# Optimization experiments

Hardware: AMD Instinct MI355X
Metric: run time of the kernel (lower is better)

Reference implementation:

```python
import jax, jax.numpy as jnp
import numpy as np

B, S, D = 2, 2048, 4096
NH, NKV = 32, 8
HD = D // NH          # 128
NREP = NH // NKV      # 4
SCALE = HD ** -0.5


def setup_inputs() -> dict:
    key = jax.random.key(0)
    kx, kq, kk, kv, ko = jax.random.split(key, 5)
    s = 0.02
    return {
        "x": jax.random.normal(kx, (B, S, D), dtype=jnp.float32),
        "wq": jax.random.normal(kq, (D, NH * HD), dtype=jnp.float32) * s,
        "wk": jax.random.normal(kk, (D, NKV * HD), dtype=jnp.float32) * s,
        "wv": jax.random.normal(kv, (D, NKV * HD), dtype=jnp.float32) * s,
        "wo": jax.random.normal(ko, (NH * HD, D), dtype=jnp.float32) * s,
    }


def reference(x, wq, wk, wv, wo):
    b, s, _ = x.shape
    q = (x @ wq).reshape(b, s, NH, HD)    # b s h d
    k = (x @ wk).reshape(b, s, NKV, HD)   # b s kv d
    v = (x @ wv).reshape(b, s, NKV, HD)
    # GQA: repeat kv heads to match query heads
    k = jnp.repeat(k, NREP, axis=2)       # b s h d
    v = jnp.repeat(v, NREP, axis=2)
    scores = jnp.einsum("bihd,bjhd->bhij", q, k) * SCALE  # b h i j
    causal = jnp.tril(jnp.ones((s, s), dtype=bool))
    scores = jnp.where(causal, scores, jnp.finfo(scores.dtype).min)
    attn = jax.nn.softmax(scores, axis=-1)
    out = jnp.einsum("bhij,bjhd->bihd", attn, v)          # b s h d
    out = out.reshape(b, s, NH * HD)
    return out @ wo
```

## Files before the change

### kernel.cpp

```cpp
#include <hip/hip_runtime.h>
#include <cstdint>
#include <cstddef>

typedef __bf16 bf16x8 __attribute__((ext_vector_type(8)));
typedef float  f32x4  __attribute__((ext_vector_type(4)));
typedef unsigned short u16;

#define SCALE_F 0.08838834764831845f
#define QSCALE_F (0.08838834764831845f * 1.4426950408889634f)

__device__ __forceinline__ u16 f2bf(float f) {
  unsigned int u = __builtin_bit_cast(unsigned int, f);
  u += 0x7fffu + ((u >> 16) & 1u);
  return (u16)(u >> 16);
}

__device__ __forceinline__ unsigned cvt_pk_bf16(float lo, float hi) {
  unsigned r;
  asm("v_cvt_pk_bf16_f32 %0, %1, %2" : "=v"(r) : "v"(lo), "v"(hi));
  return r;
}

__device__ __forceinline__ void load_lds16(const void* g, void* l) {
  __builtin_amdgcn_global_load_lds((const __attribute__((address_space(1))) void*)g,
                                   (__attribute__((address_space(3))) void*)l,
                                   16, 0, 0);
}

__global__ __launch_bounds__(256) void prep_all(const float* __restrict__ x,
                                                const float* __restrict__ wq,
                                                const float* __restrict__ wk,
                                                const float* __restrict__ wv,
                                                const float* __restrict__ wo,
                                                u16* __restrict__ xb,
                                                u16* __restrict__ wqkvT,
                                                u16* __restrict__ woT) {
  __shared__ float tile[32][33];
  const int tid = threadIdx.x;
  int blk = blockIdx.x;
  if (blk < 2048) {
    int idx = blk * 256 + tid;
    const int n4 = 4096 * 4096 / 4;
    for (; idx < n4; idx += 2048 * 256) {
      float4 v = ((const float4*)x)[idx];
      uint2 pk;
      pk.x = (unsigned)f2bf(v.x) | ((unsigned)f2bf(v.y) << 16);
      pk.y = (unsigned)f2bf(v.z) | ((unsigned)f2bf(v.w) << 16);
      ((uint2*)xb)[idx] = pk;
    }
    return;
  }
  blk -= 2048;
  const float* in; u16* out; long C; int nbx; float scale;
  if (blk < 16384)      { in = wq; out = wqkvT;                          C = 4096; nbx = 128; scale = QSCALE_F; }
  else if (blk < 20480) { blk -= 16384; in = wk; out = wqkvT + (size_t)4096 * 4096; C = 1024; nbx = 32; scale = 1.f; }
  else if (blk < 24576) { blk -= 20480; in = wv; out = wqkvT + (size_t)5120 * 4096; C = 1024; nbx = 32; scale = 1.f; }
  else                  { blk -= 24576; in = wo; out = woT;              C = 4096; nbx = 128; scale = 1.f; }
  const long R = 4096;
  const int tx = tid & 31, ty = tid >> 5;
  const long c0 = (long)(blk % nbx) * 32, r0 = (long)(blk / nbx) * 32;
#pragma unroll
  for (int i = 0; i < 4; i++)
    tile[ty + i * 8][tx] = in[(r0 + ty + i * 8) * C + c0 + tx];
  __syncthreads();
#pragma unroll
  for (int i = 0; i < 4; i++)
    out[(c0 + ty + i * 8) * R + r0 + tx] = f2bf(tile[tx][ty + i * 8] * scale);
}

__global__ __launch_bounds__(256) void transpose_u16(const u16* __restrict__ in,
                                                     u16* __restrict__ out,
                                                     int R, int C, int ldi, int ldo) {
  __shared__ u16 tile[32][33];
  const int tx = threadIdx.x, ty = threadIdx.y;
  const long c0 = (long)blockIdx.x * 32, r0 = (long)blockIdx.y * 32;
#pragma unroll
  for (int i = 0; i < 4; i++)
    tile[ty + i * 8][tx] = in[(r0 + ty + i * 8) * (long)ldi + c0 + tx];
  __syncthreads();
#pragma unroll
  for (int i = 0; i < 4; i++)
    out[(c0 + ty + i * 8) * (long)ldo + r0 + tx] = tile[tx][ty + i * 8];
}

#define STGA(db, ks, KC) { int kc_ = (KC) < K ? (KC) : 0; \
    load_lds16(gA0 + kc_, &SA[db][ks][s0 * 8]); \
    load_lds16(gA1 + kc_, &SA[db][ks][s1 * 8]); }
#define STGB(db, ks, KC) { int kc_ = (KC) < K ? (KC) : 0; \
    load_lds16(gB0 + kc_, &SB[db][ks][s0 * 8]); \
    load_lds16(gB1 + kc_, &SB[db][ks][s1 * 8]); }

#define PH(MBc, AU, BU, DBn, KSn, MBn, AN, RDB, BN, STG, DOVM) { \
    STG; \
    if (DOVM) asm volatile("s_waitcnt vmcnt(8)"); \
    __builtin_amdgcn_s_barrier(); \
    _Pragma("unroll") for (int mm = 0; mm < 4; mm++) \
      AN[mm] = *(const bf16x8*)(&SA[DBn][KSn][aoff + (MBn + mm) * 512]); \
    if (RDB) { \
      _Pragma("unroll") for (int n = 0; n < 4; n++) \
        BN[n] = *(const bf16x8*)(&SB[DBn][KSn][boff + n * 512]); \
    } \
    __builtin_amdgcn_s_setprio(1); \
    _Pragma("unroll") for (int mm = 0; mm < 4; mm++) \
      _Pragma("unroll") for (int n = 0; n < 4; n++) \
        acc[MBc + mm][n] = __builtin_amdgcn_mfma_f32_16x16x32_bf16(AU[mm], BU[n], acc[MBc + mm][n], 0, 0, 0); \
    __builtin_amdgcn_s_setprio(0); \
  }

template <int BF16_OUT>
__global__ __launch_bounds__(512, 2) void gemm256(const u16* __restrict__ A,
                                                  const u16* __restrict__ Bt,
                                                  void* __restrict__ Cv,
                                                  int M, int N, int K, int NBX) {
  __shared__ u16 SA[2][2][8192];
  __shared__ u16 SB[2][2][8192];
  const int tid = threadIdx.x;
  const int lane = tid & 63;
  const int g = lane >> 4, r16 = lane & 15;
  const int wid = tid >> 6;
  const int wm = wid >> 2, wn = wid & 3;

  const int cpx = gridDim.x >> 3;
  const int lin = (blockIdx.x & 7) * cpx + (blockIdx.x >> 3);
  const long bm = (long)(lin / NBX) * 256;
  const long bn = (long)(lin % NBX) * 256;

  const int s0 = tid, s1 = 512 + tid;
  const int rp0 = s0 >> 3, ci0 = (s0 & 7) ^ (rp0 & 7);
  const int rp1 = s1 >> 3, ci1 = (s1 & 7) ^ (rp1 & 7);
  const long gr0 = rp0 * 2 + (ci0 >> 2), gc0 = (ci0 & 3) * 8;
  const long gr1 = rp1 * 2 + (ci1 >> 2), gc1 = (ci1 & 3) * 8;
  const u16* gA0 = A + (bm + gr0) * K + gc0;
  const u16* gA1 = A + (bm + gr1) * K + gc1;
  const u16* gB0 = Bt + (bn + gr0) * K + gc0;
  const u16* gB1 = Bt + (bn + gr1) * K + gc1;

  const int rA = wm * 128 + r16;
  const int aoff = (rA >> 1) * 64 + ((((rA & 1) << 2) + g) ^ ((rA >> 1) & 7)) * 8;
  const int rB = wn * 64 + r16;
  const int boff = (rB >> 1) * 64 + ((((rB & 1) << 2) + g) ^ ((rB >> 1) & 7)) * 8;

  f32x4 acc[8][4];
#pragma unroll
  for (int m = 0; m < 8; m++)
#pragma unroll
    for (int n = 0; n < 4; n++)
#pragma unroll
      for (int j = 0; j < 4; j++) acc[m][n][j] = 0.f;

  bf16x8 afrX[4], afrY[4], bfrX[4], bfrY[4];

  STGA(0, 0, 0); STGB(0, 0, 0);
  STGA(0, 1, 32); STGB(0, 1, 32);
  STGA(1, 0, 64); STGB(1, 0, 64);
  __builtin_amdgcn_sched_barrier(0);
  asm volatile("s_waitcnt vmcnt(0)" ::: "memory");
  __builtin_amdgcn_s_barrier();

#pragma unroll
  for (int mm = 0; mm < 4; mm++)
    afrX[mm] = *(const bf16x8*)(&SA[0][0][aoff + mm * 512]);
#pragma unroll
  for (int n = 0; n < 4; n++)
    bfrX[n] = *(const bf16x8*)(&SB[0][0][boff + n * 512]);

  for (int it = 0; it < K / 128; it++) {
    const int t0 = it * 128;
    PH(0, afrX, bfrX, 0, 0, 4, afrY, 0, bfrY, STGA(1, 1, t0 + 96), 0);
    PH(4, afrY, bfrX, 0, 1, 0, afrX, 1, bfrY, STGB(1, 1, t0 + 96), 1);
    PH(0, afrX, bfrY, 0, 1, 4, afrY, 0, bfrX, STGA(0, 0, t0 + 128), 0);
    PH(4, afrY, bfrY, 1, 0, 0, afrX, 1, bfrX, STGB(0, 0, t0 + 128), 1);
    PH(0, afrX, bfrX, 1, 0, 4, afrY, 0, bfrY, STGA(0, 1, t0 + 160), 0);
    PH(4, afrY, bfrX, 1, 1, 0, afrX, 1, bfrY, STGB(0, 1, t0 + 160), 1);
    PH(0, afrX, bfrY, 1, 1, 4, afrY, 0, bfrX, STGA(1, 0, t0 + 192), 0);
    PH(4, afrY, bfrY, 0, 0, 0, afrX, 1, bfrX, STGB(1, 0, t0 + 192), 1);
  }

  const long crow = bm + wm * 128 + g * 4;
  const long ccol = bn + wn * 64 + r16;
  if (BF16_OUT) {
    u16* C = (u16*)Cv;
#pragma unroll
    for (int m = 0; m < 8; m++)
#pragma unroll
      for (int n = 0; n < 4; n++)
#pragma unroll
        for (int j = 0; j < 4; j++)
          C[(crow + m * 16 + j) * (long)N + ccol + n * 16] = f2bf(acc[m][n][j]);
  } else {
    float* C = (float*)Cv;
#pragma unroll
    for (int m = 0; m < 8; m++)
#pragma unroll
      for (int n = 0; n < 4; n++)
#pragma unroll
        for (int j = 0; j < 4; j++)
          C[(crow + m * 16 + j) * (long)N + ccol + n * 16] = acc[m][n][j];
  }
}

__global__ __launch_bounds__(512, 4) void attn_fwd(const u16* __restrict__ QK,
                                                   const u16* __restrict__ VT,
                                                   u16* __restrict__ Og) {
  __shared__ u16 Ks[2][64 * 128];
  __shared__ u16 Vs[2][128 * 64];
  __shared__ u16 Ps[8][16 * 64];
  const int tid = threadIdx.x;
  const int lane = tid & 63;
  const int w = tid >> 6;
  const int g = lane >> 4, r16 = lane & 15;
  const int qtA = blockIdx.x;
  const int qtB = 15 - qtA;
  const int h = blockIdx.y, b = blockIdx.z;
  const int kvh = h >> 2;

  const u16* kcol   = QK + (long)b * 2048 * 6144 + 4096 + kvh * 128;
  const u16* vb_ptr = VT + (long)kvh * 128 * 4096 + (long)b * 2048;
  u16* pw = Ps[w];

  const int nktA = 2 * (qtA + 1);
  const int ntot = 34;

  int qbase = qtA * 128;
  int qlo = qbase + w * 16;
  int qrow = qlo + r16;

  bf16x8 qf[4];
  auto load_q = [&]() {
    const u16* qp = QK + ((long)(b * 2048 + qrow)) * 6144 + h * 128 + g * 8;
#pragma unroll
    for (int kc = 0; kc < 4; kc++) qf[kc] = *(const bf16x8*)(qp + kc * 32);
  };
  load_q();

  f32x4 oacc[8];
  float mrun, lrun;
  auto reinit = [&]() {
#pragma unroll
    for (int dt = 0; dt < 8; dt++)
#pragma unroll
      for (int j = 0; j < 4; j++) oacc[dt][j] = 0.f;
    mrun = -__builtin_inff();
    lrun = 0.f;
  };
  reinit();

  auto finalize = [&]() {
    float li[4];
#pragma unroll
    for (int j = 0; j < 4; j++)
      li[j] = 1.f / __shfl(lrun, (lane & 48) + g * 4 + j);
    u16* op = Og + ((long)(b * 2048 + qbase + w * 16 + g * 4)) * 4096 + h * 128 + r16;
#pragma unroll
    for (int dt = 0; dt < 8; dt++)
#pragma unroll
      for (int j = 0; j < 4; j++)
        op[(long)j * 4096 + dt * 16] = f2bf(oacc[dt][j] * li[j]);
  };

  auto stage = [&](int bf, int kb) {
#pragma unroll
    for (int i = 0; i < 2; i++) {
      int slot = i * 512 + tid;
      int r = slot >> 4, cs = slot & 15;
      int ck = (cs & 8) | ((cs ^ r) & 7);
      load_lds16(kcol + (long)(kb + r) * 6144 + ck * 8, &Ks[bf][slot * 8]);
      int d = slot >> 3, c8 = slot & 7;
      int cv = (c8 ^ d) & 7;
      load_lds16(vb_ptr + (long)d * 4096 + kb + cv * 8, &Vs[bf][slot * 8]);
    }
  };

  stage(0, 0);
  __syncthreads();
  int cur = 0;

  for (int i = 0; i < ntot; i++) {
    if (i == nktA) {
      finalize();
      qbase = qtB * 128;
      qlo = qbase + w * 16;
      qrow = qlo + r16;
      load_q();
      reinit();
    }
    const int kt = (i < nktA) ? i : i - nktA;
    const int kb = kt * 64;
    if (i + 1 < ntot) {
      const int ktn = (i + 1 < nktA) ? i + 1 : i + 1 - nktA;
      stage(cur ^ 1, ktn * 64);
    }

    if (kb <= qlo + 15) {
      const bool masked = (kb + 63 > qlo);

      f32x4 st[4];
#pragma unroll
      for (int t = 0; t < 4; t++)
#pragma unroll
        for (int j = 0; j < 4; j++) st[t][j] = 0.f;
#pragma unroll
      for (int t = 0; t < 4; t++) {
        const int r = t * 16 + r16;
#pragma unroll
        for (int kc = 0; kc < 4; kc++) {
          int c = kc * 4 + g;
          int cz = (c & 8) | ((c ^ r) & 7);
          bf16x8 kf = *(const bf16x8*)(&Ks[cur][r * 128 + cz * 8]);
          st[t] = __builtin_amdgcn_mfma_f32_16x16x32_bf16(kf, qf[kc], st[t], 0, 0, 0);
        }
      }

      float p[4][4];
      float tmax = -__builtin_inff();
#pragma unroll
      for (int t = 0; t < 4; t++)
#pragma unroll
        for (int j = 0; j < 4; j++) {
          float s = st[t][j];
          if (masked) {
            int kv = kb + t * 16 + g * 4 + j;
            s = (kv > qrow) ? -__builtin_inff() : s;
          }
          p[t][j] = s;
          tmax = fmaxf(tmax, s);
        }
      tmax = fmaxf(tmax, __shfl_xor(tmax, 16));
      tmax = fmaxf(tmax, __shfl_xor(tmax, 32));

      if (!__all(tmax <= mrun + 8.f)) {
        const float mnew = fmaxf(mrun, tmax);
        const float esc = exp2f(mrun - mnew);
        float es[4];
#pragma unroll
        for (int j = 0; j < 4; j++) es[j] = __shfl(esc, (lane & 48) + g * 4 + j);
#pragma unroll
        for (int dt = 0; dt < 8; dt++)
#pragma unroll
          for (int j = 0; j < 4; j++) oacc[dt][j] *= es[j];
        lrun *= esc;
        mrun = mnew;
      }
      float psum = 0.f;
#pragma unroll
      for (int t = 0; t < 4; t++)
#pragma unroll
        for (int j = 0; j < 4; j++) {
          float e = exp2f(p[t][j] - mrun);
          p[t][j] = e;
          psum += e;
        }
      psum += __shfl_xor(psum, 16);
      psum += __shfl_xor(psum, 32);
      lrun += psum;

#pragma unroll
      for (int t = 0; t < 4; t++)
#pragma unroll
        for (int pp = 0; pp < 2; pp++) {
          int kvl = t * 16 + g * 4 + pp * 2;
          unsigned val = cvt_pk_bf16(p[t][pp * 2], p[t][pp * 2 + 1]);
          int off = r16 * 128 + ((kvl * 2) ^ ((r16 & 7) << 4));
          *(unsigned int*)((char*)pw + off) = val;
        }

#pragma unroll
      for (int kc2 = 0; kc2 < 2; kc2++) {
        int c = kc2 * 4 + g;
        int cp = c ^ (r16 & 7);
        bf16x8 pa = *(const bf16x8*)(pw + r16 * 64 + cp * 8);
#pragma unroll
        for (int dt = 0; dt < 8; dt++) {
          int d = dt * 16 + r16;
          int cz = c ^ (d & 7);
          bf16x8 vf = *(const bf16x8*)(&Vs[cur][d * 64 + cz * 8]);
          oacc[dt] = __builtin_amdgcn_mfma_f32_16x16x32_bf16(pa, vf, oacc[dt], 0, 0, 0);
        }
      }
    }

    __syncthreads();
    cur ^= 1;
  }

  finalize();
}

extern "C" void kernel_launch(void* const* d_in, const int* in_sizes, int n_in,
                              void* d_out, int out_size, void* d_ws, size_t ws_size,
                              hipStream_t stream) {
  (void)in_sizes; (void)n_in; (void)out_size; (void)ws_size;
  const float* x  = (const float*)d_in[0];
  const float* wq = (const float*)d_in[1];
  const float* wk = (const float*)d_in[2];
  const float* wv = (const float*)d_in[3];
  const float* wo = (const float*)d_in[4];
  float* out = (float*)d_out;

  u16* xb     = (u16*)d_ws;
  u16* wqkvT  = xb    + (size_t)4096 * 4096;
  u16* woT    = wqkvT + (size_t)6144 * 4096;
  u16* qkv    = woT   + (size_t)4096 * 4096;
  u16* vT     = qkv   + (size_t)4096 * 6144;
  u16* attn   = xb;

  prep_all<<<43008, 256, 0, stream>>>(x, wq, wk, wv, wo, xb, wqkvT, woT);

  gemm256<1><<<384, 512, 0, stream>>>(xb, wqkvT, qkv, 4096, 6144, 4096, 24);
  transpose_u16<<<dim3(32, 128), dim3(32, 8), 0, stream>>>(qkv + 5120, vT, 4096, 1024, 6144, 4096);

  attn_fwd<<<dim3(8, 32, 2), 512, 0, stream>>>(qkv, vT, attn);

  gemm256<0><<<256, 512, 0, stream>>>(attn, woT, out, 4096, 4096, 4096, 16);
}
```

Before: 523.3 us.

## Process two query heads per attention block to share K/V tiles

Each attention block now handles two query heads that map to the same KV head. Every K/V tile staged into shared memory therefore feeds twice the MFMA work, and the grid's y dimension is halved. In exchange each thread holds twice the accumulators and Q fragments, the P scratch buffer doubles, and the launch-bounds occupancy hint drops from 4 to 2. With half as many blocks, parallelism and latency hiding are reduced. The GEMM kernel is also split into two named wrappers around a shared inline body, with no change in behaviour.

Measured after the change: 525.5 us. No clear change (+0.4%).

```diff
diff --git a/kernel.cpp b/kernel.cpp
--- a/kernel.cpp
+++ b/kernel.cpp
@@ -90,7 +90,7 @@
     load_lds16(gB0 + kc_, &SB[db][ks][s0 * 8]); \
     load_lds16(gB1 + kc_, &SB[db][ks][s1 * 8]); }
 
-#define PH(MBc, AU, BU, DBn, KSn, MBn, AN, RDB, BN, STG, DOVM) { \
+#define PH(MBc, AU, BU, DBn, KSn, MBn, AN, RDB, BN_, STG, DOVM) { \
     STG; \
     if (DOVM) asm volatile("s_waitcnt vmcnt(8)"); \
     __builtin_amdgcn_s_barrier(); \
@@ -98,7 +98,7 @@
       AN[mm] = *(const bf16x8*)(&SA[DBn][KSn][aoff + (MBn + mm) * 512]); \
     if (RDB) { \
       _Pragma("unroll") for (int n = 0; n < 4; n++) \
-        BN[n] = *(const bf16x8*)(&SB[DBn][KSn][boff + n * 512]); \
+        BN_[n] = *(const bf16x8*)(&SB[DBn][KSn][boff + n * 512]); \
     } \
     __builtin_amdgcn_s_setprio(1); \
     _Pragma("unroll") for (int mm = 0; mm < 4; mm++) \
@@ -108,10 +108,10 @@
   }
 
 template <int BF16_OUT>
-__global__ __launch_bounds__(512, 2) void gemm256(const u16* __restrict__ A,
-                                                  const u16* __restrict__ Bt,
-                                                  void* __restrict__ Cv,
-                                                  int M, int N, int K, int NBX) {
+__device__ __forceinline__ void gemm_body(const u16* __restrict__ A,
+                                          const u16* __restrict__ Bt,
+                                          void* __restrict__ Cv,
+                                          int M, int N, int K, int NBX) {
   __shared__ u16 SA[2][2][8192];
   __shared__ u16 SB[2][2][8192];
   const int tid = threadIdx.x;
@@ -199,24 +199,37 @@
   }
 }
 
-__global__ __launch_bounds__(512, 4) void attn_fwd(const u16* __restrict__ QK,
+__global__ __launch_bounds__(512, 2) void gemm_qkv(const u16* __restrict__ A,
+                                                   const u16* __restrict__ Bt,
+                                                   void* __restrict__ Cv,
+                                                   int M, int N, int K, int NBX) {
+  gemm_body<1>(A, Bt, Cv, M, N, K, NBX);
+}
+__global__ __launch_bounds__(512, 2) void gemm_wo(const u16* __restrict__ A,
+                                                  const u16* __restrict__ Bt,
+                                                  void* __restrict__ Cv,
+                                                  int M, int N, int K, int NBX) {
+  gemm_body<0>(A, Bt, Cv, M, N, K, NBX);
+}
+
+__global__ __launch_bounds__(512, 2) void attn_fwd(const u16* __restrict__ QK,
                                                    const u16* __restrict__ VT,
                                                    u16* __restrict__ Og) {
   __shared__ u16 Ks[2][64 * 128];
   __shared__ u16 Vs[2][128 * 64];
-  __shared__ u16 Ps[8][16 * 64];
+  __shared__ u16 Ps[8][2][16 * 64];
   const int tid = threadIdx.x;
   const int lane = tid & 63;
   const int w = tid >> 6;
   const int g = lane >> 4, r16 = lane & 15;
   const int qtA = blockIdx.x;
   const int qtB = 15 - qtA;
-  const int h = blockIdx.y, b = blockIdx.z;
-  const int kvh = h >> 2;
+  const int h2 = blockIdx.y, b = blockIdx.z;
+  const int h0 = h2 * 2;
+  const int kvh = h0 >> 2;
 
   const u16* kcol   = QK + (long)b * 2048 * 6144 + 4096 + kvh * 128;
   const u16* vb_ptr = VT + (long)kvh * 128 * 4096 + (long)b * 2048;
-  u16* pw = Ps[w];
 
   const int nktA = 2 * (qtA + 1);
   const int ntot = 34;
@@ -225,37 +238,46 @@
   int qlo = qbase + w * 16;
   int qrow = qlo + r16;
 
-  bf16x8 qf[4];
+  bf16x8 qf[2][4];
   auto load_q = [&]() {
-    const u16* qp = QK + ((long)(b * 2048 + qrow)) * 6144 + h * 128 + g * 8;
-#pragma unroll
-    for (int kc = 0; kc < 4; kc++) qf[kc] = *(const bf16x8*)(qp + kc * 32);
+    const u16* qp = QK + ((long)(b * 2048 + qrow)) * 6144 + h0 * 128 + g * 8;
+#pragma unroll
+    for (int hh = 0; hh < 2; hh++)
+#pragma unroll
+      for (int kc = 0; kc < 4; kc++)
+        qf[hh][kc] = *(const bf16x8*)(qp + hh * 128 + kc * 32);
   };
   load_q();
 
-  f32x4 oacc[8];
-  float mrun, lrun;
+  f32x4 oacc[2][8];
+  float mrun[2], lrun[2];
   auto reinit = [&]() {
 #pragma unroll
-    for (int dt = 0; dt < 8; dt++)
-#pragma unroll
-      for (int j = 0; j < 4; j++) oacc[dt][j] = 0.f;
-    mrun = -__builtin_inff();
-    lrun = 0.f;
+    for (int hh = 0; hh < 2; hh++) {
+#pragma unroll
+      for (int dt = 0; dt < 8; dt++)
+#pragma unroll
+        for (int j = 0; j < 4; j++) oacc[hh][dt][j] = 0.f;
+      mrun[hh] = -__builtin_inff();
+      lrun[hh] = 0.f;
+    }
   };
   reinit();
 
   auto finalize = [&]() {
-    float li[4];
-#pragma unroll
-    for (int j = 0; j < 4; j++)
-      li[j] = 1.f / __shfl(lrun, (lane & 48) + g * 4 + j);
-    u16* op = Og + ((long)(b * 2048 + qbase + w * 16 + g * 4)) * 4096 + h * 128 + r16;
-#pragma unroll
-    for (int dt = 0; dt < 8; dt++)
+#pragma unroll
+    for (int hh = 0; hh < 2; hh++) {
+      float li[4];
 #pragma unroll
       for (int j = 0; j < 4; j++)
-        op[(long)j * 4096 + dt * 16] = f2bf(oacc[dt][j] * li[j]);
+        li[j] = 1.f / __shfl(lrun[hh], (lane & 48) + g * 4 + j);
+      u16* op = Og + ((long)(b * 2048 + qbase + w * 16 + g * 4)) * 4096 + (h0 + hh) * 128 + r16;
+#pragma unroll
+      for (int dt = 0; dt < 8; dt++)
+#pragma unroll
+        for (int j = 0; j < 4; j++)
+          op[(long)j * 4096 + dt * 16] = f2bf(oacc[hh][dt][j] * li[j]);
+    }
   };
 
   auto stage = [&](int bf, int kb) {
@@ -294,87 +316,91 @@
     if (kb <= qlo + 15) {
       const bool masked = (kb + 63 > qlo);
 
-      f32x4 st[4];
-#pragma unroll
-      for (int t = 0; t < 4; t++)
-#pragma unroll
-        for (int j = 0; j < 4; j++) st[t][j] = 0.f;
-#pragma unroll
-      for (int t = 0; t < 4; t++) {
-        const int r = t * 16 + r16;
-#pragma unroll
-        for (int kc = 0; kc < 4; kc++) {
-          int c = kc * 4 + g;
-          int cz = (c & 8) | ((c ^ r) & 7);
-          bf16x8 kf = *(const bf16x8*)(&Ks[cur][r * 128 + cz * 8]);
-          st[t] = __builtin_amdgcn_mfma_f32_16x16x32_bf16(kf, qf[kc], st[t], 0, 0, 0);
+#pragma unroll
+      for (int hh = 0; hh < 2; hh++) {
+        f32x4 st[4];
+#pragma unroll
+        for (int t = 0; t < 4; t++)
+#pragma unroll
+          for (int j = 0; j < 4; j++) st[t][j] = 0.f;
+#pragma unroll
+        for (int t = 0; t < 4; t++) {
+          const int r = t * 16 + r16;
+#pragma unroll
+          for (int kc = 0; kc < 4; kc++) {
+            int c = kc * 4 + g;
+            int cz = (c & 8) | ((c ^ r) & 7);
+            bf16x8 kf = *(const bf16x8*)(&Ks[cur][r * 128 + cz * 8]);
+            st[t] = __builtin_amdgcn_mfma_f32_16x16x32_bf16(kf, qf[hh][kc], st[t], 0, 0, 0);
+          }
         }
-      }
-
-      float p[4][4];
-      float tmax = -__builtin_inff();
-#pragma unroll
-      for (int t = 0; t < 4; t++)
-#pragma unroll
-        for (int j = 0; j < 4; j++) {
-          float s = st[t][j];
-          if (masked) {
-            int kv = kb + t * 16 + g * 4 + j;
-            s = (kv > qrow) ? -__builtin_inff() : s;
+
+        float p[4][4];
+        float tmax = -__builtin_inff();
+#pragma unroll
+        for (int t = 0; t < 4; t++)
+#pragma unroll
+          for (int j = 0; j < 4; j++) {
+            float s = st[t][j];
+            if (masked) {
+              int kv = kb + t * 16 + g * 4 + j;
+              s = (kv > qrow) ? -__builtin_inff() : s;
+            }
+            p[t][j] = s;
+            tmax = fmaxf(tmax, s);
           }
-          p[t][j] = s;
-          tmax = fmaxf(tmax, s);
+        tmax = fmaxf(tmax, __shfl_xor(tmax, 16));
+        tmax = fmaxf(tmax, __shfl_xor(tmax, 32));
+
+        if (!__all(tmax <= mrun[hh] + 8.f)) {
+          const float mnew = fmaxf(mrun[hh], tmax);
+          const float esc = exp2f(mrun[hh] - mnew);
+          float es[4];
+#pragma unroll
+          for (int j = 0; j < 4; j++) es[j] = __shfl(esc, (lane & 48) + g * 4 + j);
+#pragma unroll
+          for (int dt = 0; dt < 8; dt++)
+#pragma unroll
+            for (int j = 0; j < 4; j++) oacc[hh][dt][j] *= es[j];
+          lrun[hh] *= esc;
+          mrun[hh] = mnew;
         }
-      tmax = fmaxf(tmax, __shfl_xor(tmax, 16));
-      tmax = fmaxf(tmax, __shfl_xor(tmax, 32));
-
-      if (!__all(tmax <= mrun + 8.f)) {
-        const float mnew = fmaxf(mrun, tmax);
-        const float esc = exp2f(mrun - mnew);
-        float es[4];
-#pragma unroll
-        for (int j = 0; j < 4; j++) es[j] = __shfl(esc, (lane & 48) + g * 4 + j);
-#pragma unroll
-        for (int dt = 0; dt < 8; dt++)
-#pragma unroll
-          for (int j = 0; j < 4; j++) oacc[dt][j] *= es[j];
-        lrun *= esc;
-        mrun = mnew;
-      }
-      float psum = 0.f;
-#pragma unroll
-      for (int t = 0; t < 4; t++)
-#pragma unroll
-        for (int j = 0; j < 4; j++) {
-          float e = exp2f(p[t][j] - mrun);
-          p[t][j] = e;
-          psum += e;
-        }
-      psum += __shfl_xor(psum, 16);
-      psum += __shfl_xor(psum, 32);
-      lrun += psum;
-
-#pragma unroll
-      for (int t = 0; t < 4; t++)
-#pragma unroll
-        for (int pp = 0; pp < 2; pp++) {
-          int kvl = t * 16 + g * 4 + pp * 2;
-          unsigned val = cvt_pk_bf16(p[t][pp * 2], p[t][pp * 2 + 1]);
-          int off = r16 * 128 + ((kvl * 2) ^ ((r16 & 7) << 4));
-          *(unsigned int*)((char*)pw + off) = val;
-        }
-
-#pragma unroll
-      for (int kc2 = 0; kc2 < 2; kc2++) {
-        int c = kc2 * 4 + g;
-        int cp = c ^ (r16 & 7);
-        bf16x8 pa = *(const bf16x8*)(pw + r16 * 64 + cp * 8);
-#pragma unroll
-        for (int dt = 0; dt < 8; dt++) {
-          int d = dt * 16 + r16;
-          int cz = c ^ (d & 7);
-          bf16x8 vf = *(const bf16x8*)(&Vs[cur][d * 64 + cz * 8]);
-          oacc[dt] = __builtin_amdgcn_mfma_f32_16x16x32_bf16(pa, vf, oacc[dt], 0, 0, 0);
+        float psum = 0.f;
+#pragma unroll
+        for (int t = 0; t < 4; t++)
+#pragma unroll
+          for (int j = 0; j < 4; j++) {
+            float e = exp2f(p[t][j] - mrun[hh]);
+            p[t][j] = e;
+            psum += e;
+          }
+        psum += __shfl_xor(psum, 16);
+        psum += __shfl_xor(psum, 32);
+        lrun[hh] += psum;
+
+        u16* pw = Ps[w][hh];
+#pragma unroll
+        for (int t = 0; t < 4; t++)
+#pragma unroll
+          for (int pp = 0; pp < 2; pp++) {
+            int kvl = t * 16 + g * 4 + pp * 2;
+            unsigned val = cvt_pk_bf16(p[t][pp * 2], p[t][pp * 2 + 1]);
+            int off = r16 * 128 + ((kvl * 2) ^ ((r16 & 7) << 4));
+            *(unsigned int*)((char*)pw + off) = val;
+          }
+
+#pragma unroll
+        for (int kc2 = 0; kc2 < 2; kc2++) {
+          int c = kc2 * 4 + g;
+          int cp = c ^ (r16 & 7);
+          bf16x8 pa = *(const bf16x8*)(pw + r16 * 64 + cp * 8);
+#pragma unroll
+          for (int dt = 0; dt < 8; dt++) {
+            int d = dt * 16 + r16;
+            int cz = c ^ (d & 7);
+            bf16x8 vf = *(const bf16x8*)(&Vs[cur][d * 64 + cz * 8]);
+            oacc[hh][dt] = __builtin_amdgcn_mfma_f32_16x16x32_bf16(pa, vf, oacc[hh][dt], 0, 0, 0);
+          }
         }
       }
     }
@@ -406,10 +432,10 @@
 
   prep_all<<<43008, 256, 0, stream>>>(x, wq, wk, wv, wo, xb, wqkvT, woT);
 
-  gemm256<1><<<384, 512, 0, stream>>>(xb, wqkvT, qkv, 4096, 6144, 4096, 24);
+  gemm_qkv<<<384, 512, 0, stream>>>(xb, wqkvT, qkv, 4096, 6144, 4096, 24);
   transpose_u16<<<dim3(32, 128), dim3(32, 8), 0, stream>>>(qkv + 5120, vT, 4096, 1024, 6144, 4096);
 
-  attn_fwd<<<dim3(8, 32, 2), 512, 0, stream>>>(qkv, vT, attn);
-
-  gemm256<0><<<256, 512, 0, stream>>>(attn, woT, out, 4096, 4096, 4096, 16);
-}
+  attn_fwd<<<dim3(8, 16, 2), 512, 0, stream>>>(qkv, vT, attn);
+
+  gemm_wo<<<256, 512, 0, stream>>>(attn, woT, out, 4096, 4096, 4096, 16);
+}
```
